# Kernel tuning notes

Measured on AMD Instinct MI355X. Metric: run time of the kernel, lower is better.

## Reference

```python
import jax, jax.numpy as jnp
import numpy as np

N_DRUG = 572
EMB = 512
K_NB = 64
SEG_NB = 16
BN_EPS = 1e-5


def setup_inputs() -> dict:
    key = jax.random.key(0)
    ks = jax.random.split(key, 8)
    return {
        "drug_name": jnp.arange(N_DRUG, dtype=jnp.int64) if jax.config.jax_enable_x64 else jnp.arange(N_DRUG, dtype=jnp.int32),
        "adj_tail": jax.random.randint(ks[0], (N_DRUG, K_NB), 0, 100000),
        "adj_relation": jax.random.randint(ks[1], (N_DRUG, K_NB), 0, 200),
        "inv_adj_idx": jax.random.randint(ks[2], (N_DRUG, SEG_NB), 0, N_DRUG),
        "drug_table": jax.random.normal(ks[3], (N_DRUG, EMB), dtype=jnp.float32),
        "rela_table": jax.random.normal(ks[4], (200, EMB), dtype=jnp.float32),
        "ent_table": jax.random.normal(ks[5], (100000, EMB), dtype=jnp.float32),
        "W_lin": jax.random.normal(ks[6], (2 * EMB, EMB), dtype=jnp.float32) * (1.0 / np.sqrt(2 * EMB)),
        "b_lin": jnp.zeros((EMB,), jnp.float32),
        "bn_gamma": jnp.ones((EMB,), jnp.float32),
        "bn_beta": jnp.zeros((EMB,), jnp.float32),
        "epoch": 2,
    }


def _forward(drug_name, adj_tail, adj_relation, inv_adj_idx,
             drug_table, rela_table, ent_table, W_lin, b_lin,
             bn_gamma, bn_beta, epoch):
    # Embedding gathers
    drug_emb = drug_table[drug_name]          # [N, D]
    rel_emb = rela_table[adj_relation]        # [N, K, D]
    ent_emb = ent_table[adj_tail]             # [N, K, D]

    # KGCN-style attention over sampled neighbors: score_k = softmax(drug . rel_k)
    scores = jax.nn.softmax(jnp.einsum('nd,nkd->nk', drug_emb, rel_emb), axis=1)
    attended = jnp.einsum('nk,nkd->nd', scores, ent_emb)  # [N, D]

    # Linear -> ReLU -> BatchNorm1d (training-mode batch stats, biased var)
    e = jnp.concatenate([attended, drug_emb], axis=1)     # [N, 2D]
    h = jax.nn.relu(e @ W_lin + b_lin)                    # [N, D]
    mu = jnp.mean(h, axis=0)
    var = jnp.mean(jnp.square(h - mu), axis=0)
    drug_f = bn_gamma * (h - mu) * jax.lax.rsqrt(var + BN_EPS) + bn_beta

    if epoch > 1:
        # Sequential in-place neighbor averaging (faithful to the Python loop:
        # later drugs see already-updated rows).
        def body(f, x):
            i, pos = x
            avg = jnp.mean(f[pos], axis=0)                # [D]
            f = f.at[i].set((avg + f[i]) * 0.5)
            return f, None
        idxs = jnp.arange(N_DRUG)
        drug_f, _ = jax.lax.scan(body, drug_f, (idxs, inv_adj_idx))
    return drug_f


def reference(drug_name, adj_tail, adj_relation, inv_adj_idx,
              drug_table, rela_table, ent_table, W_lin, b_lin,
              bn_gamma, bn_beta, epoch):
    return _forward(drug_name, adj_tail, adj_relation, inv_adj_idx,
                    drug_table, rela_table, ent_table, W_lin, b_lin,
                    bn_gamma, bn_beta, epoch)
```

## Files before the change

kernel.cpp:

```cpp
#include <hip/hip_runtime.h>
#include <hip/hip_bf16.h>

#define N_DRUG 572
#define EMB    512
#define K_NB   64
#define SEG_NB 16
#define SCOLS  16
#define FPITCH 17

typedef __hip_bfloat16  bf16;
typedef __hip_bfloat162 bf162;

__device__ __forceinline__ float b2f(bf16 x){ return __bfloat162float(x); }

template<typename T> __device__ __forceinline__ float ldf(const T* p);
template<> __device__ __forceinline__ float ldf<float>(const float* p){ return *p; }
template<> __device__ __forceinline__ float ldf<bf16>(const bf16* p){ return b2f(*p); }

template<typename T> __device__ __forceinline__ float2 ld2(const T* p);
template<> __device__ __forceinline__ float2 ld2<float>(const float* p){ return *(const float2*)p; }
template<> __device__ __forceinline__ float2 ld2<bf16>(const bf16* p){
    bf162 v = *(const bf162*)p; return make_float2(b2f(v.x), b2f(v.y));
}

template<typename T> __device__ __forceinline__ void st2(T* p, float x, float y);
template<> __device__ __forceinline__ void st2<float>(float* p, float x, float y){ *(float2*)p = make_float2(x, y); }
template<> __device__ __forceinline__ void st2<bf16>(bf16* p, float x, float y){
    bf162 v; v.x = __float2bfloat16(x); v.y = __float2bfloat16(y); *(bf162*)p = v;
}

template<typename T> __device__ __forceinline__ void st1(T* p, float x);
template<> __device__ __forceinline__ void st1<float>(float* p, float x){ *p = x; }
template<> __device__ __forceinline__ void st1<bf16>(bf16* p, float x){ *p = __float2bfloat16(x); }

__device__ __forceinline__ bool idx_is64(const void* drug_name) {
    return ((const int*)drug_name)[1] == 0;
}
__device__ __forceinline__ int ld_idx(const void* p, int i, bool is64) {
    return is64 ? (int)((const long long*)p)[i] : ((const int*)p)[i];
}

__global__ void k_detect(const void* __restrict__ tab, int* __restrict__ flag)
{
    if (threadIdx.x == 0 && blockIdx.x == 0) {
        const unsigned* u = (const unsigned*)tab;
        int hits = 0;
        for (int s = 0; s < 32; ++s) {
            const unsigned e = (u[s * 997] >> 7) & 0xffu;
            hits += (e >= 110u && e <= 141u) ? 1 : 0;
        }
        *flag = (hits >= 24) ? 1 : 0;
    }
}

struct __align__(16) FwdSmem {
    float e[2][2 * EMB];
    float sc[2][K_NB];
    int   tl[2][K_NB];
};

template<typename T>
__device__ void fwd_impl(FwdSmem& sm,
    const void* drug_name, const void* adj_tail, const void* adj_rel,
    const T* __restrict__ drug_table, const T* __restrict__ rela_table,
    const T* __restrict__ ent_table,  const T* __restrict__ W,
    const T* __restrict__ bl, T* __restrict__ h)
{
    const int  t    = threadIdx.x;
    const int  n0   = blockIdx.x * 2;
    const bool is64 = idx_is64(drug_name);

    #pragma unroll
    for (int dr = 0; dr < 2; ++dr) {
        const int row = ld_idx(drug_name, n0 + dr, is64);
        const float2 v = ld2(drug_table + (size_t)row * EMB + 2 * t);
        sm.e[dr][EMB + 2 * t]     = v.x;
        sm.e[dr][EMB + 2 * t + 1] = v.y;
    }
    if (t < 128) {
        const int dr = t >> 6, k = t & 63;
        sm.tl[dr][k] = ld_idx(adj_tail, (n0 + dr) * K_NB + k, is64);
    }
    __syncthreads();

    {
        const int wave = t >> 6, lane = t & 63;
        const int dr = wave >> 1;
        const int kb = (wave & 1) * 32;
        const float* ed = &sm.e[dr][EMB];
        for (int i = 0; i < 32; ++i) {
            const int k   = kb + i;
            const int rid = ld_idx(adj_rel, (n0 + dr) * K_NB + k, is64);
            const T* rl = rela_table + (size_t)rid * EMB;
            float p = 0.f;
            #pragma unroll
            for (int m = 0; m < 4; ++m) {
                const int dd = 2 * lane + m * 128;
                const float2 rv = ld2(rl + dd);
                p = fmaf(ed[dd],     rv.x, p);
                p = fmaf(ed[dd + 1], rv.y, p);
            }
            #pragma unroll
            for (int off = 32; off; off >>= 1) p += __shfl_down(p, off, 64);
            if (lane == 0) sm.sc[dr][k] = p;
        }
    }
    __syncthreads();

    if (t < 128) {
        const int dr = t >> 6, k = t & 63;
        const float s = sm.sc[dr][k];
        float m = s;
        #pragma unroll
        for (int off = 32; off; off >>= 1) m = fmaxf(m, __shfl_xor(m, off, 64));
        const float ex = __expf(s - m);
        float sum = ex;
        #pragma unroll
        for (int off = 32; off; off >>= 1) sum += __shfl_xor(sum, off, 64);
        sm.sc[dr][k] = ex / sum;
    }
    __syncthreads();

    {
        float a00 = 0.f, a01 = 0.f, a10 = 0.f, a11 = 0.f;
        #pragma unroll 2
        for (int k = 0; k < K_NB; ++k) {
            const float w0 = sm.sc[0][k], w1 = sm.sc[1][k];
            const float2 v0 = ld2(ent_table + (size_t)sm.tl[0][k] * EMB + 2 * t);
            const float2 v1 = ld2(ent_table + (size_t)sm.tl[1][k] * EMB + 2 * t);
            a00 = fmaf(w0, v0.x, a00); a01 = fmaf(w0, v0.y, a01);
            a10 = fmaf(w1, v1.x, a10); a11 = fmaf(w1, v1.y, a11);
        }
        sm.e[0][2 * t] = a00; sm.e[0][2 * t + 1] = a01;
        sm.e[1][2 * t] = a10; sm.e[1][2 * t + 1] = a11;
    }
    __syncthreads();

    {
        const int d0 = 2 * t;
        const float2 bb = ld2(bl + d0);
        float a00 = bb.x, a01 = bb.y, a10 = bb.x, a11 = bb.y;
        const float4* E0 = (const float4*)&sm.e[0][0];
        const float4* E1 = (const float4*)&sm.e[1][0];
        #pragma unroll 2
        for (int q = 0; q < (2 * EMB) / 4; ++q) {
            const float4 f0 = E0[q];
            const float4 f1 = E1[q];
            const T* Wp = W + (size_t)(4 * q) * EMB + d0;
            const float2 w0 = ld2(Wp);
            const float2 w1 = ld2(Wp + EMB);
            const float2 w2 = ld2(Wp + 2 * EMB);
            const float2 w3 = ld2(Wp + 3 * EMB);
            a00 = fmaf(f0.x, w0.x, a00); a01 = fmaf(f0.x, w0.y, a01);
            a10 = fmaf(f1.x, w0.x, a10); a11 = fmaf(f1.x, w0.y, a11);
            a00 = fmaf(f0.y, w1.x, a00); a01 = fmaf(f0.y, w1.y, a01);
            a10 = fmaf(f1.y, w1.x, a10); a11 = fmaf(f1.y, w1.y, a11);
            a00 = fmaf(f0.z, w2.x, a00); a01 = fmaf(f0.z, w2.y, a01);
            a10 = fmaf(f1.z, w2.x, a10); a11 = fmaf(f1.z, w2.y, a11);
            a00 = fmaf(f0.w, w3.x, a00); a01 = fmaf(f0.w, w3.y, a01);
            a10 = fmaf(f1.w, w3.x, a10); a11 = fmaf(f1.w, w3.y, a11);
        }
        st2(h + (size_t)n0 * EMB + d0,       fmaxf(a00, 0.f), fmaxf(a01, 0.f));
        st2(h + (size_t)(n0 + 1) * EMB + d0, fmaxf(a10, 0.f), fmaxf(a11, 0.f));
    }
}

__global__ __launch_bounds__(256) void k_fwd(
    const int* __restrict__ flag,
    const void* drug_name, const void* adj_tail, const void* adj_rel,
    const void* drug_tab, const void* rela_tab, const void* ent_tab,
    const void* W, const void* bl, void* h)
{
    __shared__ FwdSmem sm;
    if (*flag)
        fwd_impl<bf16>(sm, drug_name, adj_tail, adj_rel,
                       (const bf16*)drug_tab, (const bf16*)rela_tab,
                       (const bf16*)ent_tab, (const bf16*)W,
                       (const bf16*)bl, (bf16*)h);
    else
        fwd_impl<float>(sm, drug_name, adj_tail, adj_rel,
                        (const float*)drug_tab, (const float*)rela_tab,
                        (const float*)ent_tab, (const float*)W,
                        (const float*)bl, (float*)h);
}

struct __align__(16) ScanSmem {
    float          fbuf[N_DRUG * FPITCH];
    unsigned short ibuf[N_DRUG * SEG_NB];
};

template<typename T>
__device__ void scan_impl(ScanSmem& sm, T* __restrict__ h, const void* inv,
    const T* __restrict__ gamma, const T* __restrict__ beta,
    const void* epoch, const void* drug_name)
{
    const int  t    = threadIdx.x;
    const int  c0   = blockIdx.x * SCOLS;
    const int  c    = t & 15, g = t >> 4;
    const bool is64 = idx_is64(drug_name);

    for (int k = t; k < N_DRUG * SEG_NB; k += 64)
        sm.ibuf[k] = (unsigned short)ld_idx(inv, k, is64);
    for (int k = t; k < N_DRUG * SCOLS; k += 64) {
        const int r = k >> 4, cc = k & 15;
        sm.fbuf[r * FPITCH + cc] = ldf(h + (size_t)r * EMB + c0 + cc);
    }
    __syncthreads();

    float s = 0.f, s2 = 0.f;
    for (int r = g; r < N_DRUG; r += 4) {
        const float x = sm.fbuf[r * FPITCH + c];
        s += x; s2 = fmaf(x, x, s2);
    }
    s  += __shfl_xor(s, 16, 64);  s  += __shfl_xor(s, 32, 64);
    s2 += __shfl_xor(s2, 16, 64); s2 += __shfl_xor(s2, 32, 64);
    const float mu  = s * (1.f / N_DRUG);
    const float var = fmaxf(s2 * (1.f / N_DRUG) - mu * mu, 0.f);
    const float gs  = ldf(gamma + c0 + c) * rsqrtf(var + 1e-5f);
    const float bs  = ldf(beta  + c0 + c);
    for (int r = g; r < N_DRUG; r += 4) {
        const float x = sm.fbuf[r * FPITCH + c];
        sm.fbuf[r * FPITCH + c] = fmaf(x - mu, gs, bs);
    }
    __syncthreads();

    if (((const int*)epoch)[0] > 1) {
        const ushort4* ip = (const ushort4*)sm.ibuf;
        ushort4 idx = ip[g];
        for (int i = 0; i < N_DRUG; ++i) {
            const int inext = (i + 1 < N_DRUG) ? i + 1 : i;
            const ushort4 nidx = ip[inext * 4 + g];
            float p = sm.fbuf[idx.x * FPITCH + c] + sm.fbuf[idx.y * FPITCH + c]
                    + sm.fbuf[idx.z * FPITCH + c] + sm.fbuf[idx.w * FPITCH + c];
            p += __shfl_xor(p, 16, 64);
            p += __shfl_xor(p, 32, 64);
            const float fi = sm.fbuf[i * FPITCH + c];
            const float nv = fmaf(p, 1.f / 32.f, fi * 0.5f);
            if (g == 0) sm.fbuf[i * FPITCH + c] = nv;
            idx = nidx;
        }
    }
    __syncthreads();

    for (int k = t; k < N_DRUG * SCOLS; k += 64) {
        const int r = k >> 4, cc = k & 15;
        st1(h + (size_t)r * EMB + c0 + cc, sm.fbuf[r * FPITCH + cc]);
    }
}

__global__ __launch_bounds__(64) void k_scan(
    const int* __restrict__ flag, void* h, const void* inv,
    const void* gamma, const void* beta, const void* epoch, const void* drug_name)
{
    __shared__ ScanSmem sm;
    if (*flag)
        scan_impl<bf16>(sm, (bf16*)h, inv, (const bf16*)gamma,
                        (const bf16*)beta, epoch, drug_name);
    else
        scan_impl<float>(sm, (float*)h, inv, (const float*)gamma,
                         (const float*)beta, epoch, drug_name);
}

extern "C" void kernel_launch(void* const* d_in, const int* in_sizes, int n_in,
                              void* d_out, int out_size, void* d_ws, size_t ws_size,
                              hipStream_t stream)
{
    (void)in_sizes; (void)n_in; (void)out_size; (void)ws_size;

    int* flag = (int*)d_ws;

    k_detect<<<1, 64, 0, stream>>>(d_in[4], flag);
    k_fwd<<<N_DRUG / 2, 256, 0, stream>>>(flag,
        d_in[0], d_in[1], d_in[2],
        d_in[4], d_in[5], d_in[6],
        d_in[7], d_in[8],
        d_out);
    k_scan<<<EMB / SCOLS, 64, 0, stream>>>(flag,
        d_out, d_in[3],
        d_in[9], d_in[10], d_in[11],
        d_in[0]);
}
```

Before: 516.8 us.

## Pipeline sequential neighbor-averaging scan with register prefetch and dependency correction

The sequential scan now gathers all 16 neighbor values per row into registers one iteration ahead. Any neighbor that equals the row being updated is fixed up with a correction term (count of self-hits times the delta), so the LDS latency of the serial chain moves off the critical path. Indices are read straight from global memory with vector loads instead of being staged in LDS, and the padded pitch is dropped. The separate dtype-detect kernel is removed: detection runs inline with a wave ballot, and loop unroll factors in the forward kernel go up. This adds register pressure and relies on the one-step correction being exact for reuse of the immediately preceding row.

```diff
diff --git a/kernel.cpp b/kernel.cpp
--- a/kernel.cpp
+++ b/kernel.cpp
@@ -6,7 +6,6 @@
 #define K_NB   64
 #define SEG_NB 16
 #define SCOLS  16
-#define FPITCH 17
 
 typedef __hip_bfloat16  bf16;
 typedef __hip_bfloat162 bf162;
@@ -40,16 +39,27 @@
     return is64 ? (int)((const long long*)p)[i] : ((const int*)p)[i];
 }
 
-__global__ void k_detect(const void* __restrict__ tab, int* __restrict__ flag)
-{
-    if (threadIdx.x == 0 && blockIdx.x == 0) {
-        const unsigned* u = (const unsigned*)tab;
-        int hits = 0;
-        for (int s = 0; s < 32; ++s) {
-            const unsigned e = (u[s * 997] >> 7) & 0xffu;
-            hits += (e >= 110u && e <= 141u) ? 1 : 0;
-        }
-        *flag = (hits >= 24) ? 1 : 0;
+__device__ __forceinline__ bool detect_bf16(const void* tab) {
+    const int lane = threadIdx.x & 63;
+    int hit = 0;
+    if (lane < 32) {
+        const unsigned u = ((const unsigned*)tab)[lane * 997];
+        const unsigned e = (u >> 7) & 0xffu;
+        hit = (e >= 110u && e <= 141u) ? 1 : 0;
+    }
+    return __popcll(__ballot(hit)) >= 24;
+}
+
+template<bool IS64>
+__device__ __forceinline__ void load_idx_row(const void* inv, int row, int idx[16]) {
+    if (IS64) {
+        const longlong2* p = (const longlong2*)inv + (size_t)row * 8;
+        #pragma unroll
+        for (int q = 0; q < 8; ++q) { longlong2 v = p[q]; idx[2*q] = (int)v.x; idx[2*q+1] = (int)v.y; }
+    } else {
+        const int4* p = (const int4*)inv + (size_t)row * 4;
+        #pragma unroll
+        for (int q = 0; q < 4; ++q) { int4 v = p[q]; idx[4*q]=v.x; idx[4*q+1]=v.y; idx[4*q+2]=v.z; idx[4*q+3]=v.w; }
     }
 }
 
@@ -88,6 +98,7 @@
         const int dr = wave >> 1;
         const int kb = (wave & 1) * 32;
         const float* ed = &sm.e[dr][EMB];
+        #pragma unroll 4
         for (int i = 0; i < 32; ++i) {
             const int k   = kb + i;
             const int rid = ld_idx(adj_rel, (n0 + dr) * K_NB + k, is64);
@@ -123,7 +134,7 @@
 
     {
         float a00 = 0.f, a01 = 0.f, a10 = 0.f, a11 = 0.f;
-        #pragma unroll 2
+        #pragma unroll 4
         for (int k = 0; k < K_NB; ++k) {
             const float w0 = sm.sc[0][k], w1 = sm.sc[1][k];
             const float2 v0 = ld2(ent_table + (size_t)sm.tl[0][k] * EMB + 2 * t);
@@ -166,13 +177,12 @@
 }
 
 __global__ __launch_bounds__(256) void k_fwd(
-    const int* __restrict__ flag,
     const void* drug_name, const void* adj_tail, const void* adj_rel,
     const void* drug_tab, const void* rela_tab, const void* ent_tab,
     const void* W, const void* bl, void* h)
 {
     __shared__ FwdSmem sm;
-    if (*flag)
+    if (detect_bf16(drug_tab))
         fwd_impl<bf16>(sm, drug_name, adj_tail, adj_rel,
                        (const bf16*)drug_tab, (const bf16*)rela_tab,
                        (const bf16*)ent_tab, (const bf16*)W,
@@ -184,32 +194,24 @@
                         (const float*)bl, (float*)h);
 }
 
-struct __align__(16) ScanSmem {
-    float          fbuf[N_DRUG * FPITCH];
-    unsigned short ibuf[N_DRUG * SEG_NB];
-};
-
-template<typename T>
-__device__ void scan_impl(ScanSmem& sm, T* __restrict__ h, const void* inv,
-    const T* __restrict__ gamma, const T* __restrict__ beta,
-    const void* epoch, const void* drug_name)
-{
-    const int  t    = threadIdx.x;
-    const int  c0   = blockIdx.x * SCOLS;
-    const int  c    = t & 15, g = t >> 4;
-    const bool is64 = idx_is64(drug_name);
-
-    for (int k = t; k < N_DRUG * SEG_NB; k += 64)
-        sm.ibuf[k] = (unsigned short)ld_idx(inv, k, is64);
+template<typename T, bool IS64>
+__device__ void scan_impl(float* __restrict__ fbuf, T* __restrict__ h,
+    const void* __restrict__ inv, const T* __restrict__ gamma,
+    const T* __restrict__ beta, const void* __restrict__ epoch)
+{
+    const int t  = threadIdx.x;
+    const int c0 = blockIdx.x * SCOLS;
+    const int c  = t & 15, g = t >> 4;
+
     for (int k = t; k < N_DRUG * SCOLS; k += 64) {
         const int r = k >> 4, cc = k & 15;
-        sm.fbuf[r * FPITCH + cc] = ldf(h + (size_t)r * EMB + c0 + cc);
+        fbuf[r * SCOLS + cc] = ldf(h + (size_t)r * EMB + c0 + cc);
     }
     __syncthreads();
 
     float s = 0.f, s2 = 0.f;
     for (int r = g; r < N_DRUG; r += 4) {
-        const float x = sm.fbuf[r * FPITCH + c];
+        const float x = fbuf[r * SCOLS + c];
         s += x; s2 = fmaf(x, x, s2);
     }
     s  += __shfl_xor(s, 16, 64);  s  += __shfl_xor(s, 32, 64);
@@ -219,64 +221,87 @@
     const float gs  = ldf(gamma + c0 + c) * rsqrtf(var + 1e-5f);
     const float bs  = ldf(beta  + c0 + c);
     for (int r = g; r < N_DRUG; r += 4) {
-        const float x = sm.fbuf[r * FPITCH + c];
-        sm.fbuf[r * FPITCH + c] = fmaf(x - mu, gs, bs);
+        const float x = fbuf[r * SCOLS + c];
+        fbuf[r * SCOLS + c] = fmaf(x - mu, gs, bs);
     }
     __syncthreads();
 
     if (((const int*)epoch)[0] > 1) {
-        const ushort4* ip = (const ushort4*)sm.ibuf;
-        ushort4 idx = ip[g];
+        int idxC[16], idxN[16];
+        float V[16], NV[16];
+
+        load_idx_row<IS64>(inv, 0, idxC);
+        #pragma unroll
+        for (int j = 0; j < 16; ++j) V[j] = fbuf[idxC[j] * SCOLS + c];
+        float fi = fbuf[c];
+        load_idx_row<IS64>(inv, 1, idxC);
+
+        float fi_p = 0.f, nv_p = 0.f, kcorr = 0.f;
+
         for (int i = 0; i < N_DRUG; ++i) {
-            const int inext = (i + 1 < N_DRUG) ? i + 1 : i;
-            const ushort4 nidx = ip[inext * 4 + g];
-            float p = sm.fbuf[idx.x * FPITCH + c] + sm.fbuf[idx.y * FPITCH + c]
-                    + sm.fbuf[idx.z * FPITCH + c] + sm.fbuf[idx.w * FPITCH + c];
-            p += __shfl_xor(p, 16, 64);
-            p += __shfl_xor(p, 32, 64);
-            const float fi = sm.fbuf[i * FPITCH + c];
-            const float nv = fmaf(p, 1.f / 32.f, fi * 0.5f);
-            if (g == 0) sm.fbuf[i * FPITCH + c] = nv;
-            idx = nidx;
+            int cn = 0;
+            #pragma unroll
+            for (int j = 0; j < 16; ++j) {
+                NV[j] = fbuf[idxC[j] * SCOLS + c];
+                cn += (idxC[j] == i) ? 1 : 0;
+            }
+            const int inx = (i + 1 < N_DRUG) ? i + 1 : N_DRUG - 1;
+            const float nfi = fbuf[inx * SCOLS + c];
+
+            float s0 = (V[0]+V[1]) + (V[2]+V[3]);
+            float s1 = (V[4]+V[5]) + (V[6]+V[7]);
+            float s2_ = (V[8]+V[9]) + (V[10]+V[11]);
+            float s3 = (V[12]+V[13]) + (V[14]+V[15]);
+            const float sum  = (s0 + s1) + (s2_ + s3);
+            const float base = fmaf(sum, 1.f / 32.f, fi * 0.5f);
+            const float nv   = fmaf(kcorr, nv_p - fi_p, base);
+
+            if (g == 0) fbuf[i * SCOLS + c] = nv;
+
+            load_idx_row<IS64>(inv, (i + 2 < N_DRUG) ? i + 2 : N_DRUG - 1, idxN);
+
+            #pragma unroll
+            for (int j = 0; j < 16; ++j) { V[j] = NV[j]; idxC[j] = idxN[j]; }
+            fi_p = fi; fi = nfi; nv_p = nv; kcorr = (float)cn * (1.f / 32.f);
         }
     }
     __syncthreads();
 
     for (int k = t; k < N_DRUG * SCOLS; k += 64) {
         const int r = k >> 4, cc = k & 15;
-        st1(h + (size_t)r * EMB + c0 + cc, sm.fbuf[r * FPITCH + cc]);
+        st1(h + (size_t)r * EMB + c0 + cc, fbuf[r * SCOLS + cc]);
     }
 }
 
 __global__ __launch_bounds__(64) void k_scan(
-    const int* __restrict__ flag, void* h, const void* inv,
-    const void* gamma, const void* beta, const void* epoch, const void* drug_name)
-{
-    __shared__ ScanSmem sm;
-    if (*flag)
-        scan_impl<bf16>(sm, (bf16*)h, inv, (const bf16*)gamma,
-                        (const bf16*)beta, epoch, drug_name);
-    else
-        scan_impl<float>(sm, (float*)h, inv, (const float*)gamma,
-                         (const float*)beta, epoch, drug_name);
+    void* h, const void* inv, const void* gamma, const void* beta,
+    const void* epoch, const void* drug_name, const void* drug_tab)
+{
+    __shared__ float fbuf[N_DRUG * SCOLS];
+    const bool isbf = detect_bf16(drug_tab);
+    const bool is64 = idx_is64(drug_name);
+    if (isbf) {
+        if (is64) scan_impl<bf16, true >(fbuf, (bf16*)h, inv, (const bf16*)gamma, (const bf16*)beta, epoch);
+        else      scan_impl<bf16, false>(fbuf, (bf16*)h, inv, (const bf16*)gamma, (const bf16*)beta, epoch);
+    } else {
+        if (is64) scan_impl<float, true >(fbuf, (float*)h, inv, (const float*)gamma, (const float*)beta, epoch);
+        else      scan_impl<float, false>(fbuf, (float*)h, inv, (const float*)gamma, (const float*)beta, epoch);
+    }
 }
 
 extern "C" void kernel_launch(void* const* d_in, const int* in_sizes, int n_in,
                               void* d_out, int out_size, void* d_ws, size_t ws_size,
                               hipStream_t stream)
 {
-    (void)in_sizes; (void)n_in; (void)out_size; (void)ws_size;
-
-    int* flag = (int*)d_ws;
-
-    k_detect<<<1, 64, 0, stream>>>(d_in[4], flag);
-    k_fwd<<<N_DRUG / 2, 256, 0, stream>>>(flag,
+    (void)in_sizes; (void)n_in; (void)out_size; (void)d_ws; (void)ws_size;
+
+    k_fwd<<<N_DRUG / 2, 256, 0, stream>>>(
         d_in[0], d_in[1], d_in[2],
         d_in[4], d_in[5], d_in[6],
         d_in[7], d_in[8],
         d_out);
-    k_scan<<<EMB / SCOLS, 64, 0, stream>>>(flag,
+    k_scan<<<EMB / SCOLS, 64, 0, stream>>>(
         d_out, d_in[3],
         d_in[9], d_in[10], d_in[11],
-        d_in[0]);
-}
+        d_in[0], d_in[4]);
+}
```

After: 757.3 us. 46.6% more time.
